# Kernel optimization log

Measured on AMD Instinct MI355X. Metric: run time of the kernel, lower is better.

Reference implementation:

```python
import jax, jax.numpy as jnp
import numpy as np

B, D_IN, H = 32768, 256, 128
N_TASK, N_EXP, N_SHARE = 2, 4, 4


def setup_inputs() -> dict:
    key = jax.random.key(0)
    ks = jax.random.split(key, 4)
    s = 1.0 / np.sqrt(D_IN)
    return {
        "x": jax.random.normal(ks[0], (B, D_IN), dtype=jnp.float32),
        "W_share": jax.random.normal(ks[1], (N_SHARE, D_IN, H), dtype=jnp.float32) * s,
        "b_share": jnp.zeros((N_SHARE, H), dtype=jnp.float32),
        "W_task": jax.random.normal(ks[2], (N_TASK, N_EXP, D_IN, H), dtype=jnp.float32) * s,
        "b_task": jnp.zeros((N_TASK, N_EXP, H), dtype=jnp.float32),
        "W_gate": jax.random.normal(ks[3], (N_TASK, D_IN, N_SHARE + N_EXP), dtype=jnp.float32) * s,
        "b_gate": jnp.zeros((N_TASK, N_SHARE + N_EXP), dtype=jnp.float32),
    }


def reference(x, W_share, b_share, W_task, b_task, W_gate, b_gate):
    # shared experts: [B, N_SHARE, H]
    share = jax.nn.relu(jnp.einsum('bd,edh->beh', x, W_share) + b_share)
    # task-specific experts: [T, B, N_EXP, H]
    task = jax.nn.relu(jnp.einsum('bd,tedh->tbeh', x, W_task) + b_task[:, None])
    # gates: [T, B, N_SHARE + N_EXP], softmax over experts
    gate = jax.nn.softmax(jnp.einsum('bd,tdg->tbg', x, W_gate) + b_gate[:, None], axis=-1)
    # concat order matches original: share_net first, then task experts
    share_b = jnp.broadcast_to(share[None], (N_TASK, B, N_SHARE, H))
    experts = jnp.concatenate([share_b, task], axis=2)  # [T, B, N_SHARE+N_EXP, H]
    towers = jnp.einsum('tbeh,tbe->tbh', experts, gate)  # [T, B, H]
    return towers
```

## Files before the change

### kernel.cpp

```cpp
#include <hip/hip_runtime.h>


typedef __attribute__((ext_vector_type(8))) short short8;
typedef __attribute__((ext_vector_type(4))) float float4v;

#define ROW_US     136
#define ROW_B      272
#define UNIT_US    17408
#define UNIT_B     34816
#define HUNIT_B    17408
#define WAVE_B     4352
#define WGT_OFF_US 417792
#define COPY_US    421888
#define COPY_B     843776

__device__ __forceinline__ unsigned short f2bf(float f) {
  unsigned u = __builtin_bit_cast(unsigned, f);
  u += 0x7FFFu + ((u >> 16) & 1u);
  return (unsigned short)(u >> 16);
}

__device__ __forceinline__ int slot2e(int sr, int t) {
  return (sr < 4) ? sr : 4 + t * 4 + (sr - 4);
}

__global__ __launch_bounds__(256)
void prep_kernel(const float* __restrict__ Ws,
                 const float* __restrict__ Wt,
                 const float* __restrict__ Wg,
                 unsigned short* __restrict__ WT, int NC) {
  int bid = blockIdx.x;
  int tid = threadIdx.x;
  if (bid < 96) {
    __shared__ float tile[64][65];
    int e  = bid >> 3;
    int kt = (bid >> 1) & 3;
    int ht = bid & 1;
    const float* src = (e < 4) ? Ws + ((size_t)e << 15)
                               : Wt + ((size_t)(e - 4) << 15);
    int m = tid & 15, n = tid >> 4;
    #pragma unroll
    for (int i = 0; i < 4; ++i) {
      int kl = i * 16 + n;
      float4 v = *(const float4*)&src[(size_t)(kt * 64 + kl) * 128 + ht * 64 + m * 4];
      tile[kl][m * 4 + 0] = v.x;
      tile[kl][m * 4 + 1] = v.y;
      tile[kl][m * 4 + 2] = v.z;
      tile[kl][m * 4 + 3] = v.w;
    }
    __syncthreads();
    #pragma unroll
    for (int i = 0; i < 4; ++i) {
      int hl = i * 16 + n;
      ushort4 o;
      o.x = f2bf(tile[m * 4 + 0][hl]);
      o.y = f2bf(tile[m * 4 + 1][hl]);
      o.z = f2bf(tile[m * 4 + 2][hl]);
      o.w = f2bf(tile[m * 4 + 3][hl]);
      size_t rowbase = (size_t)(e * 2 + (kt >> 1)) * UNIT_US
                     + (size_t)(ht * 64 + hl) * ROW_US + (kt & 1) * 64;
      for (int c = 0; c < NC; ++c) {
        *(ushort4*)&WT[(size_t)c * COPY_US + rowbase + m * 4] = o;
        if ((kt & 1) == 1 && m < 2) {
          ushort4 z = {0, 0, 0, 0};
          *(ushort4*)&WT[(size_t)c * COPY_US + rowbase + 64 + m * 4] = z;
        }
      }
    }
  } else {
    #pragma unroll
    for (int it = 0; it < 16; ++it) {
      int j = it * 256 + tid;
      int n = j >> 8, k = j & 255;
      int t = n >> 3, g = n & 7;
      unsigned short v = f2bf(Wg[(size_t)(t * 256 + k) * 8 + g]);
      for (int c = 0; c < NC; ++c)
        WT[(size_t)c * COPY_US + WGT_OFF_US + j] = v;
    }
  }
}

__global__ __launch_bounds__(256, 3)
void dmoe_main(const float* __restrict__ x,
               const unsigned short* __restrict__ WT,
               const float* __restrict__ b_share,
               const float* __restrict__ b_task,
               const float* __restrict__ b_gate,
               float* __restrict__ out, int NC) {
  __shared__ unsigned short Bs0[HUNIT_B / 2];
  __shared__ unsigned short Bs1[HUNIT_B / 2];
  __shared__ float gatesL[8 * 68];
  __shared__ float biasLds[8 * 64];

  const int tid  = threadIdx.x;
  const int lane = tid & 63;
  const int w    = tid >> 6;
  const int col  = lane & 15;
  const int quad = lane >> 4;
  const int mg   = w >> 1;
  const int ng   = w & 1;
  const int blk  = blockIdx.x;
  const int t    = blk & 1;
  const int hh   = (blk >> 1) & 1;
  const int rt   = blk >> 2;
  const int rot  = (blk >> 3) & 7;

  const char* WTc = (const char*)WT + (size_t)((blk >> 3) % NC) * COPY_B;

  uint4 p0, p1, p2, p3; unsigned p4;
  auto stageIssue = [&](int un) {
    const char* g = WTc + (size_t)un * UNIT_B + hh * HUNIT_B + w * WAVE_B;
    p0 = *(const uint4*)(g + lane * 16);
    p1 = *(const uint4*)(g + 1024 + lane * 16);
    p2 = *(const uint4*)(g + 2048 + lane * 16);
    p3 = *(const uint4*)(g + 3072 + lane * 16);
    p4 = *(const unsigned*)(g + 4096 + lane * 4);
  };
  auto deposit = [&](unsigned short* dst) {
    char* l = (char*)dst + w * WAVE_B;
    *(uint4*)(l + lane * 16)        = p0;
    *(uint4*)(l + 1024 + lane * 16) = p1;
    *(uint4*)(l + 2048 + lane * 16) = p2;
    *(uint4*)(l + 3072 + lane * 16) = p3;
    *(unsigned*)(l + 4096 + lane * 4) = p4;
  };

  const int e0 = slot2e(rot, t);
  stageIssue(e0 * 2);

  short8 A[2][8];
  {
    const float* xb = x + ((size_t)rt * 64 + mg * 32 + col) * 256 + quad * 8;
    #pragma unroll
    for (int mt = 0; mt < 2; ++mt) {
      const float* xr = xb + (size_t)mt * 16 * 256;
      #pragma unroll
      for (int k = 0; k < 8; ++k) {
        float4v u = *(const float4v*)(xr + k * 32);
        float4v v = *(const float4v*)(xr + k * 32 + 4);
        short8 fr;
        fr[0] = (short)f2bf(u[0]); fr[1] = (short)f2bf(u[1]);
        fr[2] = (short)f2bf(u[2]); fr[3] = (short)f2bf(u[3]);
        fr[4] = (short)f2bf(v[0]); fr[5] = (short)f2bf(v[1]);
        fr[6] = (short)f2bf(v[2]); fr[7] = (short)f2bf(v[3]);
        A[mt][k] = fr;
        asm volatile("" : "+a"(A[mt][k]));
      }
    }
  }

  deposit(Bs0);

  for (int i = tid; i < 512; i += 256) {
    int sr = i >> 6, hl = i & 63, h = hh * 64 + hl;
    biasLds[i] = (sr < 4) ? b_share[sr * 128 + h]
                          : b_task[(size_t)(t * 4 + (sr - 4)) * 128 + h];
  }

  {
    const unsigned short* WgT = (const unsigned short*)(WTc + WGT_OFF_US * 2);
    const int gr = col & 7;
    const unsigned short* bp = WgT + (size_t)(t * 8 + gr) * 256 + quad * 8;
    float bg = b_gate[t * 8 + gr];
    float4v ag[2] = {{0.f,0.f,0.f,0.f},{0.f,0.f,0.f,0.f}};
    #pragma unroll
    for (int kb = 0; kb < 2; ++kb) {
      short8 Bg[4];
      #pragma unroll
      for (int j = 0; j < 4; ++j) Bg[j] = *(const short8*)(bp + (kb * 4 + j) * 32);
      #pragma unroll
      for (int j = 0; j < 4; ++j) {
        ag[0] = __builtin_amdgcn_mfma_f32_16x16x32_bf16(A[0][kb * 4 + j], Bg[j], ag[0], 0, 0, 0);
        ag[1] = __builtin_amdgcn_mfma_f32_16x16x32_bf16(A[1][kb * 4 + j], Bg[j], ag[1], 0, 0, 0);
      }
    }
    #pragma unroll
    for (int mt = 0; mt < 2; ++mt) {
      #pragma unroll
      for (int r = 0; r < 4; ++r) {
        float vlog = ag[mt][r] + bg;
        float m = vlog;
        m = fmaxf(m, __shfl_xor(m, 1));
        m = fmaxf(m, __shfl_xor(m, 2));
        m = fmaxf(m, __shfl_xor(m, 4));
        float p = __expf(vlog - m);
        float s = p;
        s += __shfl_xor(s, 1);
        s += __shfl_xor(s, 2);
        s += __shfl_xor(s, 4);
        if (ng == 0 && col < 8)
          gatesL[col * 68 + mg * 32 + mt * 16 + quad * 4 + r] = p / s;
      }
    }
  }
  __syncthreads();

  float tw[2][2][4];
  #pragma unroll
  for (int mt = 0; mt < 2; ++mt)
    #pragma unroll
    for (int nt = 0; nt < 2; ++nt)
      #pragma unroll
      for (int r = 0; r < 4; ++r)
        tw[mt][nt][r] = 0.f;

  const int hb = ng * 32;
  float4v acc[2][2];

  #pragma unroll 1
  for (int s = 0; s < 8; ++s) {
    const int sr  = (s + rot) & 7;
    const int e   = slot2e(sr, t);
    const int e2  = slot2e((s + 1 + rot) & 7, t);
    #pragma unroll
    for (int kh = 0; kh < 2; ++kh) {
      const bool doStage = !(s == 7 && kh == 1);
      if (doStage) stageIssue(kh == 0 ? e * 2 + 1 : e2 * 2);
      if (kh == 0) {
        #pragma unroll
        for (int mt = 0; mt < 2; ++mt)
          #pragma unroll
          for (int nt = 0; nt < 2; ++nt)
            acc[mt][nt] = (float4v){0.f, 0.f, 0.f, 0.f};
      }
      {
        const char* Bb = (const char*)(kh ? Bs1 : Bs0);
        __builtin_amdgcn_s_setprio(1);
        #pragma unroll
        for (int kk = 0; kk < 4; ++kk) {
          #pragma unroll
          for (int nt = 0; nt < 2; ++nt) {
            short8 bfr = *(const short8*)(Bb + (hb + nt * 16 + col) * ROW_B
                                          + kk * 64 + quad * 16);
            acc[0][nt] = __builtin_amdgcn_mfma_f32_16x16x32_bf16(
                A[0][kh * 4 + kk], bfr, acc[0][nt], 0, 0, 0);
            acc[1][nt] = __builtin_amdgcn_mfma_f32_16x16x32_bf16(
                A[1][kh * 4 + kk], bfr, acc[1][nt], 0, 0, 0);
          }
        }
        __builtin_amdgcn_s_setprio(0);
      }
      if (doStage) deposit(kh ? Bs0 : Bs1);
      if (kh == 1) {
        #pragma unroll
        for (int mt = 0; mt < 2; ++mt) {
          int rb = mg * 32 + mt * 16 + quad * 4;
          float4 g = *(const float4*)&gatesL[sr * 68 + rb];
          #pragma unroll
          for (int nt = 0; nt < 2; ++nt) {
            float bias = biasLds[sr * 64 + hb + nt * 16 + col];
            #pragma unroll
            for (int r = 0; r < 4; ++r) {
              float v = fmaxf(acc[mt][nt][r] + bias, 0.f);
              tw[mt][nt][r] += ((const float*)&g)[r] * v;
            }
          }
        }
      }
      __syncthreads();
    }
  }

  #pragma unroll
  for (int mt = 0; mt < 2; ++mt)
    #pragma unroll
    for (int r = 0; r < 4; ++r) {
      size_t row = (size_t)rt * 64 + mg * 32 + mt * 16 + quad * 4 + r;
      float* op = out + ((size_t)t << 22) + row * 128 + hh * 64 + hb;
      #pragma unroll
      for (int nt = 0; nt < 2; ++nt)
        __builtin_nontemporal_store(tw[mt][nt][r], op + nt * 16 + col);
    }
}

extern "C" void kernel_launch(void* const* d_in, const int* in_sizes, int n_in,
                              void* d_out, int out_size, void* d_ws, size_t ws_size,
                              hipStream_t stream) {
  const float* x       = (const float*)d_in[0];
  const float* W_share = (const float*)d_in[1];
  const float* b_share = (const float*)d_in[2];
  const float* W_task  = (const float*)d_in[3];
  const float* b_task  = (const float*)d_in[4];
  const float* W_gate  = (const float*)d_in[5];
  const float* b_gate  = (const float*)d_in[6];
  float* out = (float*)d_out;
  unsigned short* WT = (unsigned short*)d_ws;

  int NC = (int)(ws_size / (size_t)COPY_B);
  if (NC < 1) NC = 1;
  if (NC > 2) NC = 2;

  prep_kernel<<<97, 256, 0, stream>>>(W_share, W_task, W_gate, WT, NC);
  dmoe_main<<<2048, 256, 0, stream>>>(x, WT, b_share, b_task, b_gate, out, NC);
}
```

Measured before the change: 170.7 us.

## Stage expert weights via direct global-to-LDS loads with XOR swizzle, 32-row tiles

Replaces the register-staged weight copy (load to VGPRs, then write to LDS) with global_load_lds direct transfers of full 128-column weight units. The padded row layout is replaced by an XOR-swizzled layout to avoid LDS bank conflicts. Each block now covers 32 rows across all 128 output columns instead of 64 rows by 64 columns, which doubles LDS per block and drops occupancy to 2 blocks. The intent is to cut VGPR pressure and staging instructions, at the cost of each block re-reading the full weight set for fewer rows, i.e. more weight traffic per row processed.

```diff
diff --git a/kernel.cpp b/kernel.cpp
--- a/kernel.cpp
+++ b/kernel.cpp
@@ -4,15 +4,13 @@
 typedef __attribute__((ext_vector_type(8))) short short8;
 typedef __attribute__((ext_vector_type(4))) float float4v;
 
-#define ROW_US     136
-#define ROW_B      272
-#define UNIT_US    17408
-#define UNIT_B     34816
-#define HUNIT_B    17408
-#define WAVE_B     4352
-#define WGT_OFF_US 417792
-#define COPY_US    421888
-#define COPY_B     843776
+#define ROW_US     128
+#define ROW_B      256
+#define UNIT_US    16384
+#define UNIT_B     32768
+#define WGT_OFF_US 393216
+#define COPY_US    397312
+#define COPY_B     794624
 
 __device__ __forceinline__ unsigned short f2bf(float f) {
   unsigned u = __builtin_bit_cast(unsigned, f);
@@ -22,6 +20,12 @@
 
 __device__ __forceinline__ int slot2e(int sr, int t) {
   return (sr < 4) ? sr : 4 + t * 4 + (sr - 4);
+}
+
+typedef const __attribute__((address_space(1))) unsigned int GBUF;
+typedef __attribute__((address_space(3))) unsigned int LBUF;
+__device__ __forceinline__ void gll16(const void* g, void* l) {
+  __builtin_amdgcn_global_load_lds((GBUF*)g, (LBUF*)l, 16, 0, 0);
 }
 
 __global__ __launch_bounds__(256)
@@ -57,15 +61,11 @@
       o.y = f2bf(tile[m * 4 + 1][hl]);
       o.z = f2bf(tile[m * 4 + 2][hl]);
       o.w = f2bf(tile[m * 4 + 3][hl]);
-      size_t rowbase = (size_t)(e * 2 + (kt >> 1)) * UNIT_US
-                     + (size_t)(ht * 64 + hl) * ROW_US + (kt & 1) * 64;
-      for (int c = 0; c < NC; ++c) {
-        *(ushort4*)&WT[(size_t)c * COPY_US + rowbase + m * 4] = o;
-        if ((kt & 1) == 1 && m < 2) {
-          ushort4 z = {0, 0, 0, 0};
-          *(ushort4*)&WT[(size_t)c * COPY_US + rowbase + 64 + m * 4] = z;
-        }
-      }
+      int kofs = (((kt & 1) * 64) + m * 4) ^ ((hl & 7) << 3);
+      size_t base = (size_t)(e * 2 + (kt >> 1)) * UNIT_US
+                  + (size_t)(ht * 64 + hl) * ROW_US + kofs;
+      for (int c = 0; c < NC; ++c)
+        *(ushort4*)&WT[(size_t)c * COPY_US + base] = o;
     }
   } else {
     #pragma unroll
@@ -80,57 +80,44 @@
   }
 }
 
-__global__ __launch_bounds__(256, 3)
+__global__ __launch_bounds__(256, 2)
 void dmoe_main(const float* __restrict__ x,
                const unsigned short* __restrict__ WT,
                const float* __restrict__ b_share,
                const float* __restrict__ b_task,
                const float* __restrict__ b_gate,
                float* __restrict__ out, int NC) {
-  __shared__ unsigned short Bs0[HUNIT_B / 2];
-  __shared__ unsigned short Bs1[HUNIT_B / 2];
-  __shared__ float gatesL[8 * 68];
-  __shared__ float biasLds[8 * 64];
+  __shared__ unsigned short Bs0[UNIT_US];
+  __shared__ unsigned short Bs1[UNIT_US];
+  __shared__ float gatesL[8 * 36];
+  __shared__ float biasLds[8 * 128];
 
   const int tid  = threadIdx.x;
   const int lane = tid & 63;
   const int w    = tid >> 6;
   const int col  = lane & 15;
   const int quad = lane >> 4;
-  const int mg   = w >> 1;
-  const int ng   = w & 1;
   const int blk  = blockIdx.x;
   const int t    = blk & 1;
-  const int hh   = (blk >> 1) & 1;
-  const int rt   = blk >> 2;
+  const int rt   = blk >> 1;
   const int rot  = (blk >> 3) & 7;
 
   const char* WTc = (const char*)WT + (size_t)((blk >> 3) % NC) * COPY_B;
 
-  uint4 p0, p1, p2, p3; unsigned p4;
-  auto stageIssue = [&](int un) {
-    const char* g = WTc + (size_t)un * UNIT_B + hh * HUNIT_B + w * WAVE_B;
-    p0 = *(const uint4*)(g + lane * 16);
-    p1 = *(const uint4*)(g + 1024 + lane * 16);
-    p2 = *(const uint4*)(g + 2048 + lane * 16);
-    p3 = *(const uint4*)(g + 3072 + lane * 16);
-    p4 = *(const unsigned*)(g + 4096 + lane * 4);
+  auto stage = [&](int un, unsigned short* dst) {
+    const char* g = WTc + (size_t)un * UNIT_B + w * 8192;
+    char* l = (char*)dst + w * 8192;
+    #pragma unroll
+    for (int i = 0; i < 8; ++i)
+      gll16(g + i * 1024 + lane * 16, l + i * 1024);
   };
-  auto deposit = [&](unsigned short* dst) {
-    char* l = (char*)dst + w * WAVE_B;
-    *(uint4*)(l + lane * 16)        = p0;
-    *(uint4*)(l + 1024 + lane * 16) = p1;
-    *(uint4*)(l + 2048 + lane * 16) = p2;
-    *(uint4*)(l + 3072 + lane * 16) = p3;
-    *(unsigned*)(l + 4096 + lane * 4) = p4;
-  };
 
   const int e0 = slot2e(rot, t);
-  stageIssue(e0 * 2);
+  stage(e0 * 2, Bs0);
 
   short8 A[2][8];
   {
-    const float* xb = x + ((size_t)rt * 64 + mg * 32 + col) * 256 + quad * 8;
+    const float* xb = x + ((size_t)rt * 32 + col) * 256 + quad * 8;
     #pragma unroll
     for (int mt = 0; mt < 2; ++mt) {
       const float* xr = xb + (size_t)mt * 16 * 256;
@@ -149,10 +136,8 @@
     }
   }
 
-  deposit(Bs0);
-
-  for (int i = tid; i < 512; i += 256) {
-    int sr = i >> 6, hl = i & 63, h = hh * 64 + hl;
+  for (int i = tid; i < 1024; i += 256) {
+    int sr = i >> 7, h = i & 127;
     biasLds[i] = (sr < 4) ? b_share[sr * 128 + h]
                           : b_task[(size_t)(t * 4 + (sr - 4)) * 128 + h];
   }
@@ -188,8 +173,8 @@
         s += __shfl_xor(s, 1);
         s += __shfl_xor(s, 2);
         s += __shfl_xor(s, 4);
-        if (ng == 0 && col < 8)
-          gatesL[col * 68 + mg * 32 + mt * 16 + quad * 4 + r] = p / s;
+        if (w == 0 && col < 8)
+          gatesL[col * 36 + mt * 16 + quad * 4 + r] = p / s;
       }
     }
   }
@@ -204,7 +189,8 @@
       for (int r = 0; r < 4; ++r)
         tw[mt][nt][r] = 0.f;
 
-  const int hb = ng * 32;
+  const int hb = w * 32;
+  const int c7 = col & 7;
   float4v acc[2][2];
 
   #pragma unroll 1
@@ -215,7 +201,7 @@
     #pragma unroll
     for (int kh = 0; kh < 2; ++kh) {
       const bool doStage = !(s == 7 && kh == 1);
-      if (doStage) stageIssue(kh == 0 ? e * 2 + 1 : e2 * 2);
+      if (doStage) stage(kh == 0 ? e * 2 + 1 : e2 * 2, kh ? Bs0 : Bs1);
       if (kh == 0) {
         #pragma unroll
         for (int mt = 0; mt < 2; ++mt)
@@ -231,7 +217,7 @@
           #pragma unroll
           for (int nt = 0; nt < 2; ++nt) {
             short8 bfr = *(const short8*)(Bb + (hb + nt * 16 + col) * ROW_B
-                                          + kk * 64 + quad * 16);
+                                          + ((((kk << 2) + quad) ^ c7) << 4));
             acc[0][nt] = __builtin_amdgcn_mfma_f32_16x16x32_bf16(
                 A[0][kh * 4 + kk], bfr, acc[0][nt], 0, 0, 0);
             acc[1][nt] = __builtin_amdgcn_mfma_f32_16x16x32_bf16(
@@ -240,15 +226,13 @@
         }
         __builtin_amdgcn_s_setprio(0);
       }
-      if (doStage) deposit(kh ? Bs0 : Bs1);
       if (kh == 1) {
         #pragma unroll
         for (int mt = 0; mt < 2; ++mt) {
-          int rb = mg * 32 + mt * 16 + quad * 4;
-          float4 g = *(const float4*)&gatesL[sr * 68 + rb];
+          float4 g = *(const float4*)&gatesL[sr * 36 + mt * 16 + quad * 4];
           #pragma unroll
           for (int nt = 0; nt < 2; ++nt) {
-            float bias = biasLds[sr * 64 + hb + nt * 16 + col];
+            float bias = biasLds[sr * 128 + hb + nt * 16 + col];
             #pragma unroll
             for (int r = 0; r < 4; ++r) {
               float v = fmaxf(acc[mt][nt][r] + bias, 0.f);
@@ -265,8 +249,8 @@
   for (int mt = 0; mt < 2; ++mt)
     #pragma unroll
     for (int r = 0; r < 4; ++r) {
-      size_t row = (size_t)rt * 64 + mg * 32 + mt * 16 + quad * 4 + r;
-      float* op = out + ((size_t)t << 22) + row * 128 + hh * 64 + hb;
+      size_t row = (size_t)rt * 32 + mt * 16 + quad * 4 + r;
+      float* op = out + ((size_t)t << 22) + row * 128 + hb;
       #pragma unroll
       for (int nt = 0; nt < 2; ++nt)
         __builtin_nontemporal_store(tw[mt][nt][r], op + nt * 16 + col);
```

Result: slower. 177.2 us (+3.8%).
